# Kernel tuning notes

Measured on AMD Instinct MI355X. Metric: run time of the kernel, lower is better.

The kernel has to match this reference:

```python
import jax, jax.numpy as jnp
import numpy as np
from jax import lax

EPS = 1e-5  # BatchNorm1d default eps

def setup_inputs() -> dict:
    key = jax.random.key(0)
    ks = jax.random.split(key, 8)
    B, IN, H, T = 1024, 128, 256, 256
    return {
        "inputs": jax.random.normal(ks[0], (B, IN), jnp.float32),
        "hidden": jnp.zeros((B, H), jnp.float32),
        "W_ih": jax.random.normal(ks[1], (3 * H, IN), jnp.float32) * 0.05,
        "b_ih": jax.random.normal(ks[2], (3 * H,), jnp.float32) * 0.05,
        "W_hh": jax.random.normal(ks[3], (3 * H, H), jnp.float32) * 0.05,
        "b_hh": jax.random.normal(ks[4], (3 * H,), jnp.float32) * 0.05,
        "W_lin": jax.random.normal(ks[5], (IN, H), jnp.float32) * 0.05,
        "b_lin": jax.random.normal(ks[6], (IN,), jnp.float32) * 0.05,
        "n_frames": 256,
    }

def reference(inputs, hidden, W_ih, b_ih, W_hh, b_hh, W_lin, b_lin, n_frames):
    def step(carry, _):
        x, h = carry
        gi = x @ W_ih.T + b_ih          # [B, 3H]
        gh = h @ W_hh.T + b_hh          # [B, 3H]
        i_r, i_z, i_n = jnp.split(gi, 3, axis=-1)
        h_r, h_z, h_n = jnp.split(gh, 3, axis=-1)
        r = jax.nn.sigmoid(i_r + h_r)
        z = jax.nn.sigmoid(i_z + h_z)
        n = jnp.tanh(i_n + r * h_n)
        h_new = (1.0 - z) * n + z * h   # GRUCell update
        y = h_new @ W_lin.T + b_lin     # fed back as next input
        return (y, h_new), y

    _, ys = lax.scan(step, (inputs, hidden), None, length=n_frames)  # [T, B, out]
    # BatchNorm1d(affine=False), training mode: biased batch stats per timestep
    mean = jnp.mean(ys, axis=1, keepdims=True)
    var = jnp.var(ys, axis=1, keepdims=True)
    return (ys - mean) / jnp.sqrt(var + EPS)
```

## Files before the change

### kernel.cpp

```cpp
#include <hip/hip_runtime.h>


typedef _Float16 half8 __attribute__((ext_vector_type(8)));
typedef float floatx4 __attribute__((ext_vector_type(4)));
typedef unsigned uintx4 __attribute__((ext_vector_type(4)));

#define EPS_BN 1e-5f

#define WS_WC 0
#define WS_W0 524288
#define WS_WL 1114112
#define WS_B0 1179648
#define WS_BC 1183744

static __device__ __forceinline__ unsigned short f2h(float f) {
    union { _Float16 h; unsigned short u; } v;
    v.h = (_Float16)f;
    return v.u;
}
static __device__ __forceinline__ unsigned pack2h(float a, float b) {
    return (unsigned)f2h(a) | ((unsigned)f2h(b) << 16);
}
static __device__ __forceinline__ float2 up2(unsigned u) {
    union { unsigned v; _Float16 h[2]; } x; x.v = u;
    return make_float2((float)x.h[0], (float)x.h[1]);
}
static __device__ __forceinline__ half8 as_h8(uint4 v) {
    union { uint4 u; half8 h; } x; x.u = v; return x.h;
}
static __device__ __forceinline__ half8 ld_agpr(const uint4* p) {
    uintx4 v = *(const uintx4*)p;
    asm volatile("; wpin" : "+a"(v));
    union { uintx4 u; half8 h; } x; x.u = v; return x.h;
}
static __device__ __forceinline__ float sigm(float x) {
    return __builtin_amdgcn_rcpf(1.0f + __builtin_amdgcn_exp2f(-1.442695041f * x));
}
static __device__ __forceinline__ float tanh_fast(float x) {
    return 1.0f - 2.0f * __builtin_amdgcn_rcpf(1.0f + __builtin_amdgcn_exp2f(2.885390082f * x));
}
static __device__ __forceinline__ void bar_lgkm() {
    asm volatile("s_waitcnt lgkmcnt(0)\n\ts_barrier" ::: "memory");
}
#define MFMA16(A, B, C) __builtin_amdgcn_mfma_f32_16x16x32_f16((A), (B), (C), 0, 0, 0)

__global__ void pack_all_kernel(const float* __restrict__ W_ih, const float* __restrict__ W_hh,
                                const float* __restrict__ W_lin, const float* __restrict__ b_ih,
                                const float* __restrict__ b_hh, const float* __restrict__ b_lin,
                                uint4* __restrict__ w0, uint4* __restrict__ wl,
                                float4* __restrict__ bias0,
                                uint4* __restrict__ wc, float4* __restrict__ bc)
{
    __shared__ float sh[256][8];
    if (blockIdx.x < 161) {
        int i = blockIdx.x * 256 + threadIdx.x;
        if (i < 36864) {
            int lane = i & 63, tile = i >> 6;
            int w = tile / 36, rem = tile - w * 36;
            int g = rem / 12, kt = rem - g * 12;
            int n = g * 256 + (w << 4) + (lane & 15);
            int k0 = (kt << 5) + ((lane >> 4) << 3);
            const float* p = (k0 < 128) ? (W_ih + n * 128 + k0)
                                        : (W_hh + n * 256 + (k0 - 128));
            unsigned short h[8];
            #pragma unroll
            for (int j = 0; j < 8; ++j) h[j] = f2h(p[j]);
            uint4 v;
            v.x = (unsigned)h[0] | ((unsigned)h[1] << 16);
            v.y = (unsigned)h[2] | ((unsigned)h[3] << 16);
            v.z = (unsigned)h[4] | ((unsigned)h[5] << 16);
            v.w = (unsigned)h[6] | ((unsigned)h[7] << 16);
            w0[i] = v;
        } else if (i < 40960) {
            int i2 = i - 36864;
            int lane = i2 & 63, tile = i2 >> 6;
            int n = (tile >> 3) * 16 + (lane & 15);
            int k0 = ((tile & 7) << 5) + ((lane >> 4) << 3);
            const float* p = W_lin + n * 256 + k0;
            unsigned short h[8];
            #pragma unroll
            for (int j = 0; j < 8; ++j) h[j] = f2h(p[j]);
            uint4 v;
            v.x = (unsigned)h[0] | ((unsigned)h[1] << 16);
            v.y = (unsigned)h[2] | ((unsigned)h[3] << 16);
            v.z = (unsigned)h[4] | ((unsigned)h[5] << 16);
            v.w = (unsigned)h[6] | ((unsigned)h[7] << 16);
            wl[i2] = v;
        } else if (i < 41216) {
            int cb = i - 40960;
            bias0[cb] = make_float4(b_ih[cb] + b_hh[cb],
                                    b_ih[256 + cb] + b_hh[256 + cb],
                                    b_ih[512 + cb], b_hh[512 + cb]);
        }
        return;
    }
    int i = (blockIdx.x - 161) * 256 + threadIdx.x;
    if (i < 65536) {
        const int tid  = threadIdx.x;
        const int lane = i & 63;
        const int half = (i >> 6) & 1;
        const int tile = i >> 7;
        int w = tile >> 5, r = tile & 31;
        int g = r >> 3, kt = r & 7;
        int c = (w << 4) + (lane & 15);
        int k0 = (kt << 5) + ((lane >> 4) << 3);
        float s[8];
        #pragma unroll
        for (int j = 0; j < 8; ++j) s[j] = 0.0f;
        if (g == 3) {
            if (half == 0) {
                #pragma unroll
                for (int j = 0; j < 8; ++j) s[j] = W_hh[(512 + c) * 256 + k0 + j];
            }
        } else {
            int row = g * 256 + c;
            const float* wi = W_ih + row * 128 + (half << 6);
            for (int ii = 0; ii < 64; ++ii) {
                float wv = wi[ii];
                const float* wrow = W_lin + ((half << 6) + ii) * 256 + k0;
                #pragma unroll
                for (int j = 0; j < 8; ++j) s[j] += wv * wrow[j];
            }
            if (g < 2 && half == 0) {
                #pragma unroll
                for (int j = 0; j < 8; ++j) s[j] += W_hh[row * 256 + k0 + j];
            }
        }
        #pragma unroll
        for (int j = 0; j < 8; ++j) sh[tid][j] = s[j];
        __syncthreads();
        if (half == 0) {
            #pragma unroll
            for (int j = 0; j < 8; ++j) s[j] += sh[tid + 64][j];
            unsigned short h[8];
            #pragma unroll
            for (int j = 0; j < 8; ++j) h[j] = f2h(s[j]);
            uint4 v;
            v.x = (unsigned)h[0] | ((unsigned)h[1] << 16);
            v.y = (unsigned)h[2] | ((unsigned)h[3] << 16);
            v.z = (unsigned)h[4] | ((unsigned)h[5] << 16);
            v.w = (unsigned)h[6] | ((unsigned)h[7] << 16);
            wc[tile * 64 + lane] = v;
        }
    } else if (i < 65792) {
        int c = i - 65536;
        float d0 = 0.f, d1 = 0.f, d2 = 0.f;
        for (int ii = 0; ii < 128; ++ii) {
            float bl = b_lin[ii];
            d0 += bl * W_ih[c * 128 + ii];
            d1 += bl * W_ih[(256 + c) * 128 + ii];
            d2 += bl * W_ih[(512 + c) * 128 + ii];
        }
        bc[c] = make_float4(b_ih[c] + b_hh[c] + d0,
                            b_ih[256 + c] + b_hh[256 + c] + d1,
                            b_ih[512 + c] + d2,
                            b_hh[512 + c]);
    }
}

__global__ __launch_bounds__(512, 2) void gru_kernel(
    const float* __restrict__ inputs,
    const float* __restrict__ hidden,
    const uint4* __restrict__ wc,
    const uint4* __restrict__ w0,
    const float4* __restrict__ bias0,
    const float4* __restrict__ bcp,
    float* __restrict__ out)
{
    __shared__ uint4 lds[9472];

    const int tid  = threadIdx.x;
    const int lane = tid & 63;
    const int w    = tid >> 6;
    const int quad = lane >> 4;
    const int nc   = lane & 15;
    const int r0   = blockIdx.x << 4;
    const int c0   = (w << 4) + nc;
    const int c1   = 128 + c0;
    const float4 bc0 = bcp[c0];
    const float4 bc1 = bcp[c1];
    const uint4* wcw0 = wc + (size_t)w * 2048;
    const uint4* wcw1 = wc + (size_t)(w + 8) * 2048;

    half8 wr0[8], wz0[8], wr1[8], wz1[8];
    #pragma unroll
    for (int kt = 0; kt < 8; ++kt) {
        wr0[kt] = ld_agpr(&wcw0[kt * 64 + lane]);
        wz0[kt] = ld_agpr(&wcw0[(8 + kt) * 64 + lane]);
        wr1[kt] = ld_agpr(&wcw1[kt * 64 + lane]);
        wz1[kt] = ld_agpr(&wcw1[(8 + kt) * 64 + lane]);
    }

    const int wbase = 1280 + (w << 10);
    #pragma unroll
    for (int i = 0; i < 4; ++i) {
        lds[wbase + (i << 6) + lane]             = wcw0[(16 + i) * 64 + lane];
        lds[wbase + ((4 + i) << 6) + lane]       = wcw0[(24 + i) * 64 + lane];
        lds[wbase + 512 + (i << 6) + lane]       = wcw1[(16 + i) * 64 + lane];
        lds[wbase + 512 + ((4 + i) << 6) + lane] = wcw1[(24 + i) * 64 + lane];
    }

    float hreg[8];
    #pragma unroll
    for (int d = 0; d < 4; ++d) {
        hreg[d]     = hidden[(r0 + (quad << 2) + d) * 256 + c0];
        hreg[4 + d] = hidden[(r0 + (quad << 2) + d) * 256 + c1];
    }

    unsigned short* lds_u16 = (unsigned short*)lds;
    const int kp  = ((w & 1) << 4) + nc;
    const int lf  = ((kp >> 3) << 4) + (quad << 2);
    const int hfb0 = (((w >> 1) * 64 + lf) << 3) + (kp & 7);
    const int hfb1 = (((4 + (w >> 1)) * 64 + lf) << 3) + (kp & 7);

    for (int idx = tid; idx < 2048; idx += 512) {
        int ktl = idx >> 8;
        int rem = idx & 255;
        int lfr = rem >> 2, jg = rem & 3;
        int m = lfr & 15;
        int hc = ktl * 32 + (lfr >> 4) * 8 + jg * 2;
        const float* p = hidden + (r0 + m) * 256 + hc;
        unsigned pk = (unsigned)f2h(p[0]) | ((unsigned)f2h(p[1]) << 16);
        ((unsigned*)lds)[(ktl * 64 + lfr) * 4 + jg] = pk;
    }
    for (int idx = tid; idx < 1024; idx += 512) {
        int kt = idx >> 8, lfr = (idx >> 2) & 63, jg = idx & 3;
        int m = lfr & 15;
        int k0 = (kt << 5) + ((lfr >> 4) << 3) + (jg << 1);
        const float* p = inputs + (r0 + m) * 128 + k0;
        unsigned pk = (unsigned)f2h(p[0]) | ((unsigned)f2h(p[1]) << 16);
        ((unsigned*)lds)[(1024 + (kt << 6) + lfr) * 4 + jg] = pk;
    }
    __syncthreads();

    unsigned short* Hout = (unsigned short*)out;

    {
        #pragma unroll
        for (int g2 = 0; g2 < 2; ++g2) {
            const uint4* ww = w0 + (size_t)(g2 ? (w + 8) : w) * 2304;
            floatx4 ar = {0.f,0.f,0.f,0.f}, az = {0.f,0.f,0.f,0.f};
            floatx4 ain = {0.f,0.f,0.f,0.f}, ahn = {0.f,0.f,0.f,0.f};
            #pragma unroll
            for (int kt = 0; kt < 12; ++kt) {
                half8 A = as_h8(kt < 4 ? lds[1024 + (kt << 6) + lane]
                                       : lds[((kt - 4) << 6) + lane]);
                ar = MFMA16(A, as_h8(ww[kt * 64 + lane]), ar);
                az = MFMA16(A, as_h8(ww[(12 + kt) * 64 + lane]), az);
                if (kt < 4)
                    ain = MFMA16(A, as_h8(ww[(24 + kt) * 64 + lane]), ain);
                else
                    ahn = MFMA16(A, as_h8(ww[(24 + kt) * 64 + lane]), ahn);
            }
            const int cc = g2 ? c1 : c0;
            const int hfb = g2 ? hfb1 : hfb0;
            float4 b0 = bias0[cc];
            #pragma unroll
            for (int d = 0; d < 4; ++d) {
                float rr = sigm(ar[d] + b0.x);
                float zz = sigm(az[d] + b0.y);
                float nn = tanh_fast(ain[d] + b0.z + rr * (ahn[d] + b0.w));
                float hnew = (1.0f - zz) * nn + zz * hreg[(g2 << 2) + d];
                hreg[(g2 << 2) + d] = hnew;
                unsigned short hu = f2h(hnew);
                lds_u16[4096 + hfb + (d << 3)] = hu;
                Hout[((size_t)(r0 + (quad << 2) + d) << 8) + cc] = hu;
            }
        }
        bar_lgkm();
    }

    for (int t = 1; t < 256; ++t) {
        const int rb   = (t & 1) << 9;
        const int wb16 = (((t + 1) & 1) << 9) << 3;

        const uint4* s0p = wcw0 + lane;
        const uint4* s1p = wcw1 + lane;
        asm("" : "+v"(s0p), "+v"(s1p));

        uint4 si0[4], sh0[4], si1[4], sh1[4];
        si0[0] = s0p[20 * 64]; sh0[0] = s0p[28 * 64];
        si1[0] = s1p[20 * 64]; sh1[0] = s1p[28 * 64];

        floatx4 ar0 = {0.f,0.f,0.f,0.f}, az0 = {0.f,0.f,0.f,0.f};
        floatx4 ai0 = {0.f,0.f,0.f,0.f}, ah0 = {0.f,0.f,0.f,0.f};
        floatx4 ar1 = {0.f,0.f,0.f,0.f}, az1 = {0.f,0.f,0.f,0.f};
        floatx4 ai1 = {0.f,0.f,0.f,0.f}, ah1 = {0.f,0.f,0.f,0.f};

        #pragma unroll
        for (int kt = 0; kt < 8; ++kt) {
            half8 A = as_h8(lds[rb + (kt << 6) + lane]);
            if (kt == 1) {
                si0[1] = s0p[21 * 64]; sh0[1] = s0p[29 * 64];
                si1[1] = s1p[21 * 64]; sh1[1] = s1p[29 * 64];
            }
            if (kt == 2) {
                si0[2] = s0p[22 * 64]; sh0[2] = s0p[30 * 64];
                si1[2] = s1p[22 * 64]; sh1[2] = s1p[30 * 64];
            }
            if (kt == 3) {
                si0[3] = s0p[23 * 64]; sh0[3] = s0p[31 * 64];
                si1[3] = s1p[23 * 64]; sh1[3] = s1p[31 * 64];
            }
            ar0 = MFMA16(A, wr0[kt], ar0);
            ar1 = MFMA16(A, wr1[kt], ar1);
            az0 = MFMA16(A, wz0[kt], az0);
            az1 = MFMA16(A, wz1[kt], az1);
            half8 Bi0 = (kt < 4) ? as_h8(lds[wbase + (kt << 6) + lane])
                                 : as_h8(si0[kt - 4]);
            half8 Bi1 = (kt < 4) ? as_h8(lds[wbase + 512 + (kt << 6) + lane])
                                 : as_h8(si1[kt - 4]);
            ai0 = MFMA16(A, Bi0, ai0);
            ai1 = MFMA16(A, Bi1, ai1);
            half8 Bh0 = (kt < 4) ? as_h8(lds[wbase + ((4 + kt) << 6) + lane])
                                 : as_h8(sh0[kt - 4]);
            half8 Bh1 = (kt < 4) ? as_h8(lds[wbase + 512 + ((4 + kt) << 6) + lane])
                                 : as_h8(sh1[kt - 4]);
            ah0 = MFMA16(A, Bh0, ah0);
            ah1 = MFMA16(A, Bh1, ah1);
        }

        const size_t obase = (size_t)t * 1024 + r0 + (quad << 2);
        #pragma unroll
        for (int d = 0; d < 4; ++d) {
            float rr = sigm(ar0[d] + bc0.x);
            float zz = sigm(az0[d] + bc0.y);
            float nn = tanh_fast(ai0[d] + bc0.z + rr * (ah0[d] + bc0.w));
            float hnew = (1.0f - zz) * nn + zz * hreg[d];
            hreg[d] = hnew;
            unsigned short hu = f2h(hnew);
            lds_u16[wb16 + hfb0 + (d << 3)] = hu;
            Hout[((obase + d) << 8) + c0] = hu;
        }
        #pragma unroll
        for (int d = 0; d < 4; ++d) {
            float rr = sigm(ar1[d] + bc1.x);
            float zz = sigm(az1[d] + bc1.y);
            float nn = tanh_fast(ai1[d] + bc1.z + rr * (ah1[d] + bc1.w));
            float hnew = (1.0f - zz) * nn + zz * hreg[4 + d];
            hreg[4 + d] = hnew;
            unsigned short hu = f2h(hnew);
            lds_u16[wb16 + hfb1 + (d << 3)] = hu;
            Hout[((obase + d) << 8) + c1] = hu;
        }
        bar_lgkm();
    }
}

__global__ __launch_bounds__(512, 2) void yfused_kernel(
    const uint4* __restrict__ wl, const float* __restrict__ b_lin,
    float* __restrict__ out)
{
    __shared__ uint4 bfr[4096];
    __shared__ float sred[8][256];
    __shared__ float snorm[256];

    const int tid  = threadIdx.x;
    const int lane = tid & 63;
    const int w    = tid >> 6;
    const int quad = lane >> 4;
    const int nc   = lane & 15;
    const int t    = blockIdx.x;

    const unsigned short* H = (const unsigned short*)out + (size_t)t * 262144;
    float* Y = out + (size_t)t * 131072;

    #pragma unroll
    for (int i = 0; i < 8; ++i)
        bfr[(i << 9) + tid] = wl[(i << 9) + tid];

    float blv[8];
    #pragma unroll
    for (int c = 0; c < 8; ++c) blv[c] = b_lin[(c << 4) + nc];

    __syncthreads();

    const int rw0 = w << 7;
    float s1[8], s2[8];
    #pragma unroll
    for (int c = 0; c < 8; ++c) { s1[c] = 0.f; s2[c] = 0.f; }
    uintx4 ypk[32];

    #pragma unroll
    for (int s = 0; s < 8; ++s) {
        const unsigned short* hrow = H + (size_t)(rw0 + (s << 4) + nc) * 256 + (quad << 3);
        uint4 A[8];
        #pragma unroll
        for (int kt = 0; kt < 8; ++kt)
            A[kt] = *(const uint4*)(hrow + (kt << 5));
        unsigned te0 = 0, te1 = 0;
        #pragma unroll
        for (int c = 0; c < 8; ++c) {
            floatx4 acc = {0.f, 0.f, 0.f, 0.f};
            #pragma unroll
            for (int kt = 0; kt < 8; ++kt)
                acc = MFMA16(as_h8(A[kt]), as_h8(bfr[(((c << 3) + kt) << 6) + lane]), acc);
            float y0 = acc[0] + blv[c], y1 = acc[1] + blv[c];
            float y2 = acc[2] + blv[c], y3 = acc[3] + blv[c];
            s1[c] += (y0 + y1) + (y2 + y3);
            s2[c] += (y0 * y0 + y1 * y1) + (y2 * y2 + y3 * y3);
            unsigned q0 = pack2h(y0, y1), q1 = pack2h(y2, y3);
            if ((c & 1) == 0) { te0 = q0; te1 = q1; }
            else {
                uintx4 v; v[0] = te0; v[1] = te1; v[2] = q0; v[3] = q1;
                asm volatile("; ypin" : "+a"(v));
                ypk[(s << 2) + (c >> 1)] = v;
            }
        }
    }

    #pragma unroll
    for (int c = 0; c < 8; ++c) {
        s1[c] += __shfl_xor(s1[c], 16); s1[c] += __shfl_xor(s1[c], 32);
        s2[c] += __shfl_xor(s2[c], 16); s2[c] += __shfl_xor(s2[c], 32);
    }
    if (lane < 16) {
        #pragma unroll
        for (int c = 0; c < 8; ++c) {
            sred[w][(c << 4) + lane]       = s1[c];
            sred[w][128 + (c << 4) + lane] = s2[c];
        }
    }
    __syncthreads();
    if (tid < 128) {
        float a1 = 0.f, a2 = 0.f;
        #pragma unroll
        for (int w2 = 0; w2 < 8; ++w2) {
            a1 += sred[w2][tid];
            a2 += sred[w2][128 + tid];
        }
        float mean = a1 * (1.0f / 1024.0f);
        float var  = a2 * (1.0f / 1024.0f) - mean * mean;
        snorm[tid]       = mean;
        snorm[128 + tid] = rsqrtf(var + EPS_BN);
    }
    __syncthreads();

    float mn[8], scl[8];
    #pragma unroll
    for (int c = 0; c < 8; ++c) {
        mn[c]  = snorm[(c << 4) + nc];
        scl[c] = snorm[128 + (c << 4) + nc];
    }

    #pragma unroll
    for (int s = 0; s < 8; ++s) {
        float* yrow = Y + (size_t)(rw0 + (s << 4) + (quad << 2)) * 128 + nc;
        #pragma unroll
        for (int cp = 0; cp < 4; ++cp) {
            uintx4 v = ypk[(s << 2) + cp];
            const int c0 = cp << 1, c1 = c0 + 1;
            float2 a01 = up2(v[0]), a23 = up2(v[1]);
            float2 b01 = up2(v[2]), b23 = up2(v[3]);
            const int o0 = cp << 5, o1 = o0 + 16;
            yrow[0 * 128 + o0] = (a01.x - mn[c0]) * scl[c0];
            yrow[1 * 128 + o0] = (a01.y - mn[c0]) * scl[c0];
            yrow[2 * 128 + o0] = (a23.x - mn[c0]) * scl[c0];
            yrow[3 * 128 + o0] = (a23.y - mn[c0]) * scl[c0];
            yrow[0 * 128 + o1] = (b01.x - mn[c1]) * scl[c1];
            yrow[1 * 128 + o1] = (b01.y - mn[c1]) * scl[c1];
            yrow[2 * 128 + o1] = (b23.x - mn[c1]) * scl[c1];
            yrow[3 * 128 + o1] = (b23.y - mn[c1]) * scl[c1];
        }
    }
}

extern "C" void kernel_launch(void* const* d_in, const int* in_sizes, int n_in,
                              void* d_out, int out_size, void* d_ws, size_t ws_size,
                              hipStream_t stream) {
    (void)in_sizes; (void)n_in; (void)out_size; (void)ws_size;
    const float* inputs = (const float*)d_in[0];
    const float* hidden = (const float*)d_in[1];
    const float* W_ih   = (const float*)d_in[2];
    const float* b_ih   = (const float*)d_in[3];
    const float* W_hh   = (const float*)d_in[4];
    const float* b_hh   = (const float*)d_in[5];
    const float* W_lin  = (const float*)d_in[6];
    const float* b_lin  = (const float*)d_in[7];

    char* ws = (char*)d_ws;
    uint4*  wcp   = (uint4*)(ws + WS_WC);
    uint4*  w0p   = (uint4*)(ws + WS_W0);
    uint4*  wlp   = (uint4*)(ws + WS_WL);
    float4* bias0 = (float4*)(ws + WS_B0);
    float4* bcp   = (float4*)(ws + WS_BC);

    pack_all_kernel<<<418, 256, 0, stream>>>(W_ih, W_hh, W_lin, b_ih, b_hh, b_lin,
                                             w0p, wlp, bias0, wcp, bcp);
    gru_kernel<<<64, 512, 0, stream>>>(inputs, hidden, wcp, w0p, bias0, bcp, (float*)d_out);
    yfused_kernel<<<256, 512, 0, stream>>>(wlp, b_lin, (float*)d_out);
}
```

Baseline: 1.003 ms.

## Split GRU recurrence across 16 waves per block, one column group each

The recurrent GRU kernel goes from 512 to 1024 threads per block. Each of the 16 waves now owns a single 16-column group instead of two, so the per-wave register-resident weights, the LDS-staged weights, the MFMA chains and the gate epilogue all halve. The goal is to shorten the serial per-timestep critical path on each wave by exposing more wave-level parallelism inside the latency-bound recurrence. The cost is more waves meeting at the per-step barrier and possibly higher contention on LDS and the MFMA units within a CU.

```diff
diff --git a/kernel.cpp b/kernel.cpp
--- a/kernel.cpp
+++ b/kernel.cpp
@@ -158,7 +158,7 @@
     }
 }
 
-__global__ __launch_bounds__(512, 2) void gru_kernel(
+__global__ __launch_bounds__(1024, 4) void gru_kernel(
     const float* __restrict__ inputs,
     const float* __restrict__ hidden,
     const uint4* __restrict__ wc,
@@ -176,44 +176,34 @@
     const int nc   = lane & 15;
     const int r0   = blockIdx.x << 4;
     const int c0   = (w << 4) + nc;
-    const int c1   = 128 + c0;
     const float4 bc0 = bcp[c0];
-    const float4 bc1 = bcp[c1];
-    const uint4* wcw0 = wc + (size_t)w * 2048;
-    const uint4* wcw1 = wc + (size_t)(w + 8) * 2048;
-
-    half8 wr0[8], wz0[8], wr1[8], wz1[8];
+    const uint4* wcw = wc + (size_t)w * 2048;
+
+    half8 wr[8], wz[8];
     #pragma unroll
     for (int kt = 0; kt < 8; ++kt) {
-        wr0[kt] = ld_agpr(&wcw0[kt * 64 + lane]);
-        wz0[kt] = ld_agpr(&wcw0[(8 + kt) * 64 + lane]);
-        wr1[kt] = ld_agpr(&wcw1[kt * 64 + lane]);
-        wz1[kt] = ld_agpr(&wcw1[(8 + kt) * 64 + lane]);
-    }
-
-    const int wbase = 1280 + (w << 10);
+        wr[kt] = ld_agpr(&wcw[kt * 64 + lane]);
+        wz[kt] = ld_agpr(&wcw[(8 + kt) * 64 + lane]);
+    }
+
+    const int wbase = 1280 + (w << 9);
     #pragma unroll
     for (int i = 0; i < 4; ++i) {
-        lds[wbase + (i << 6) + lane]             = wcw0[(16 + i) * 64 + lane];
-        lds[wbase + ((4 + i) << 6) + lane]       = wcw0[(24 + i) * 64 + lane];
-        lds[wbase + 512 + (i << 6) + lane]       = wcw1[(16 + i) * 64 + lane];
-        lds[wbase + 512 + ((4 + i) << 6) + lane] = wcw1[(24 + i) * 64 + lane];
-    }
-
-    float hreg[8];
-    #pragma unroll
-    for (int d = 0; d < 4; ++d) {
-        hreg[d]     = hidden[(r0 + (quad << 2) + d) * 256 + c0];
-        hreg[4 + d] = hidden[(r0 + (quad << 2) + d) * 256 + c1];
-    }
+        lds[wbase + (i << 6) + lane]       = wcw[(16 + i) * 64 + lane];
+        lds[wbase + ((4 + i) << 6) + lane] = wcw[(24 + i) * 64 + lane];
+    }
+
+    float hreg[4];
+    #pragma unroll
+    for (int d = 0; d < 4; ++d)
+        hreg[d] = hidden[(r0 + (quad << 2) + d) * 256 + c0];
 
     unsigned short* lds_u16 = (unsigned short*)lds;
     const int kp  = ((w & 1) << 4) + nc;
     const int lf  = ((kp >> 3) << 4) + (quad << 2);
     const int hfb0 = (((w >> 1) * 64 + lf) << 3) + (kp & 7);
-    const int hfb1 = (((4 + (w >> 1)) * 64 + lf) << 3) + (kp & 7);
-
-    for (int idx = tid; idx < 2048; idx += 512) {
+
+    for (int idx = tid; idx < 2048; idx += 1024) {
         int ktl = idx >> 8;
         int rem = idx & 255;
         int lfr = rem >> 2, jg = rem & 3;
@@ -223,7 +213,8 @@
         unsigned pk = (unsigned)f2h(p[0]) | ((unsigned)f2h(p[1]) << 16);
         ((unsigned*)lds)[(ktl * 64 + lfr) * 4 + jg] = pk;
     }
-    for (int idx = tid; idx < 1024; idx += 512) {
+    if (tid < 1024) {
+        int idx = tid;
         int kt = idx >> 8, lfr = (idx >> 2) & 63, jg = idx & 3;
         int m = lfr & 15;
         int k0 = (kt << 5) + ((lfr >> 4) << 3) + (jg << 1);
@@ -236,36 +227,31 @@
     unsigned short* Hout = (unsigned short*)out;
 
     {
-        #pragma unroll
-        for (int g2 = 0; g2 < 2; ++g2) {
-            const uint4* ww = w0 + (size_t)(g2 ? (w + 8) : w) * 2304;
-            floatx4 ar = {0.f,0.f,0.f,0.f}, az = {0.f,0.f,0.f,0.f};
-            floatx4 ain = {0.f,0.f,0.f,0.f}, ahn = {0.f,0.f,0.f,0.f};
-            #pragma unroll
-            for (int kt = 0; kt < 12; ++kt) {
-                half8 A = as_h8(kt < 4 ? lds[1024 + (kt << 6) + lane]
-                                       : lds[((kt - 4) << 6) + lane]);
-                ar = MFMA16(A, as_h8(ww[kt * 64 + lane]), ar);
-                az = MFMA16(A, as_h8(ww[(12 + kt) * 64 + lane]), az);
-                if (kt < 4)
-                    ain = MFMA16(A, as_h8(ww[(24 + kt) * 64 + lane]), ain);
-                else
-                    ahn = MFMA16(A, as_h8(ww[(24 + kt) * 64 + lane]), ahn);
-            }
-            const int cc = g2 ? c1 : c0;
-            const int hfb = g2 ? hfb1 : hfb0;
-            float4 b0 = bias0[cc];
-            #pragma unroll
-            for (int d = 0; d < 4; ++d) {
-                float rr = sigm(ar[d] + b0.x);
-                float zz = sigm(az[d] + b0.y);
-                float nn = tanh_fast(ain[d] + b0.z + rr * (ahn[d] + b0.w));
-                float hnew = (1.0f - zz) * nn + zz * hreg[(g2 << 2) + d];
-                hreg[(g2 << 2) + d] = hnew;
-                unsigned short hu = f2h(hnew);
-                lds_u16[4096 + hfb + (d << 3)] = hu;
-                Hout[((size_t)(r0 + (quad << 2) + d) << 8) + cc] = hu;
-            }
+        const uint4* ww = w0 + (size_t)w * 2304;
+        floatx4 ar = {0.f,0.f,0.f,0.f}, az = {0.f,0.f,0.f,0.f};
+        floatx4 ain = {0.f,0.f,0.f,0.f}, ahn = {0.f,0.f,0.f,0.f};
+        #pragma unroll
+        for (int kt = 0; kt < 12; ++kt) {
+            half8 A = as_h8(kt < 4 ? lds[1024 + (kt << 6) + lane]
+                                   : lds[((kt - 4) << 6) + lane]);
+            ar = MFMA16(A, as_h8(ww[kt * 64 + lane]), ar);
+            az = MFMA16(A, as_h8(ww[(12 + kt) * 64 + lane]), az);
+            if (kt < 4)
+                ain = MFMA16(A, as_h8(ww[(24 + kt) * 64 + lane]), ain);
+            else
+                ahn = MFMA16(A, as_h8(ww[(24 + kt) * 64 + lane]), ahn);
+        }
+        float4 b0 = bias0[c0];
+        #pragma unroll
+        for (int d = 0; d < 4; ++d) {
+            float rr = sigm(ar[d] + b0.x);
+            float zz = sigm(az[d] + b0.y);
+            float nn = tanh_fast(ain[d] + b0.z + rr * (ahn[d] + b0.w));
+            float hnew = (1.0f - zz) * nn + zz * hreg[d];
+            hreg[d] = hnew;
+            unsigned short hu = f2h(hnew);
+            lds_u16[4096 + hfb0 + (d << 3)] = hu;
+            Hout[((size_t)(r0 + (quad << 2) + d) << 8) + c0] = hu;
         }
         bar_lgkm();
     }
@@ -274,74 +260,42 @@
         const int rb   = (t & 1) << 9;
         const int wb16 = (((t + 1) & 1) << 9) << 3;
 
-        const uint4* s0p = wcw0 + lane;
-        const uint4* s1p = wcw1 + lane;
-        asm("" : "+v"(s0p), "+v"(s1p));
-
-        uint4 si0[4], sh0[4], si1[4], sh1[4];
-        si0[0] = s0p[20 * 64]; sh0[0] = s0p[28 * 64];
-        si1[0] = s1p[20 * 64]; sh1[0] = s1p[28 * 64];
-
-        floatx4 ar0 = {0.f,0.f,0.f,0.f}, az0 = {0.f,0.f,0.f,0.f};
-        floatx4 ai0 = {0.f,0.f,0.f,0.f}, ah0 = {0.f,0.f,0.f,0.f};
-        floatx4 ar1 = {0.f,0.f,0.f,0.f}, az1 = {0.f,0.f,0.f,0.f};
-        floatx4 ai1 = {0.f,0.f,0.f,0.f}, ah1 = {0.f,0.f,0.f,0.f};
+        const uint4* sp = wcw + lane;
+        asm("" : "+v"(sp));
+
+        uint4 si[4], sh[4];
+        si[0] = sp[20 * 64]; sh[0] = sp[28 * 64];
+
+        floatx4 ar = {0.f,0.f,0.f,0.f}, az = {0.f,0.f,0.f,0.f};
+        floatx4 ai = {0.f,0.f,0.f,0.f}, ah = {0.f,0.f,0.f,0.f};
 
         #pragma unroll
         for (int kt = 0; kt < 8; ++kt) {
             half8 A = as_h8(lds[rb + (kt << 6) + lane]);
-            if (kt == 1) {
-                si0[1] = s0p[21 * 64]; sh0[1] = s0p[29 * 64];
-                si1[1] = s1p[21 * 64]; sh1[1] = s1p[29 * 64];
-            }
-            if (kt == 2) {
-                si0[2] = s0p[22 * 64]; sh0[2] = s0p[30 * 64];
-                si1[2] = s1p[22 * 64]; sh1[2] = s1p[30 * 64];
-            }
-            if (kt == 3) {
-                si0[3] = s0p[23 * 64]; sh0[3] = s0p[31 * 64];
-                si1[3] = s1p[23 * 64]; sh1[3] = s1p[31 * 64];
-            }
-            ar0 = MFMA16(A, wr0[kt], ar0);
-            ar1 = MFMA16(A, wr1[kt], ar1);
-            az0 = MFMA16(A, wz0[kt], az0);
-            az1 = MFMA16(A, wz1[kt], az1);
-            half8 Bi0 = (kt < 4) ? as_h8(lds[wbase + (kt << 6) + lane])
-                                 : as_h8(si0[kt - 4]);
-            half8 Bi1 = (kt < 4) ? as_h8(lds[wbase + 512 + (kt << 6) + lane])
-                                 : as_h8(si1[kt - 4]);
-            ai0 = MFMA16(A, Bi0, ai0);
-            ai1 = MFMA16(A, Bi1, ai1);
-            half8 Bh0 = (kt < 4) ? as_h8(lds[wbase + ((4 + kt) << 6) + lane])
-                                 : as_h8(sh0[kt - 4]);
-            half8 Bh1 = (kt < 4) ? as_h8(lds[wbase + 512 + ((4 + kt) << 6) + lane])
-                                 : as_h8(sh1[kt - 4]);
-            ah0 = MFMA16(A, Bh0, ah0);
-            ah1 = MFMA16(A, Bh1, ah1);
+            if (kt == 1) { si[1] = sp[21 * 64]; sh[1] = sp[29 * 64]; }
+            if (kt == 2) { si[2] = sp[22 * 64]; sh[2] = sp[30 * 64]; }
+            if (kt == 3) { si[3] = sp[23 * 64]; sh[3] = sp[31 * 64]; }
+            ar = MFMA16(A, wr[kt], ar);
+            az = MFMA16(A, wz[kt], az);
+            half8 Bi = (kt < 4) ? as_h8(lds[wbase + (kt << 6) + lane])
+                                : as_h8(si[kt - 4]);
+            ai = MFMA16(A, Bi, ai);
+            half8 Bh = (kt < 4) ? as_h8(lds[wbase + ((4 + kt) << 6) + lane])
+                                : as_h8(sh[kt - 4]);
+            ah = MFMA16(A, Bh, ah);
         }
 
         const size_t obase = (size_t)t * 1024 + r0 + (quad << 2);
         #pragma unroll
         for (int d = 0; d < 4; ++d) {
-            float rr = sigm(ar0[d] + bc0.x);
-            float zz = sigm(az0[d] + bc0.y);
-            float nn = tanh_fast(ai0[d] + bc0.z + rr * (ah0[d] + bc0.w));
+            float rr = sigm(ar[d] + bc0.x);
+            float zz = sigm(az[d] + bc0.y);
+            float nn = tanh_fast(ai[d] + bc0.z + rr * (ah[d] + bc0.w));
             float hnew = (1.0f - zz) * nn + zz * hreg[d];
             hreg[d] = hnew;
             unsigned short hu = f2h(hnew);
             lds_u16[wb16 + hfb0 + (d << 3)] = hu;
             Hout[((obase + d) << 8) + c0] = hu;
-        }
-        #pragma unroll
-        for (int d = 0; d < 4; ++d) {
-            float rr = sigm(ar1[d] + bc1.x);
-            float zz = sigm(az1[d] + bc1.y);
-            float nn = tanh_fast(ai1[d] + bc1.z + rr * (ah1[d] + bc1.w));
-            float hnew = (1.0f - zz) * nn + zz * hreg[4 + d];
-            hreg[4 + d] = hnew;
-            unsigned short hu = f2h(hnew);
-            lds_u16[wb16 + hfb1 + (d << 3)] = hu;
-            Hout[((obase + d) << 8) + c1] = hu;
         }
         bar_lgkm();
     }
@@ -487,6 +441,6 @@
 
     pack_all_kernel<<<418, 256, 0, stream>>>(W_ih, W_hh, W_lin, b_ih, b_hh, b_lin,
                                              w0p, wlp, bias0, wcp, bcp);
-    gru_kernel<<<64, 512, 0, stream>>>(inputs, hidden, wcp, w0p, bias0, bcp, (float*)d_out);
+    gru_kernel<<<64, 1024, 0, stream>>>(inputs, hidden, wcp, w0p, bias0, bcp, (float*)d_out);
     yfused_kernel<<<256, 512, 0, stream>>>(wlp, b_lin, (float*)d_out);
 }
```

Measured after the change: 854.4 us. 14.8% less time.
